# Kernel optimization log

Measured on AMD Instinct MI355X. Metric: run time of the kernel, lower is better.

Reference implementation:

```python
import jax, jax.numpy as jnp
import numpy as np

B, T, D = 8, 2048, 512


def setup_inputs() -> dict:
    key = jax.random.key(0)
    ks = jax.random.split(key, 12)
    s = 1.0 / np.sqrt(D)
    return {
        "x": jax.random.normal(ks[0], (B, T, D), dtype=jnp.float32),
        "Wq": jax.random.normal(ks[1], (D, D), dtype=jnp.float32) * s,
        "bq": jax.random.normal(ks[2], (D,), dtype=jnp.float32) * 0.01,
        "Wk": jax.random.normal(ks[3], (D, D), dtype=jnp.float32) * s,
        "bk": jax.random.normal(ks[4], (D,), dtype=jnp.float32) * 0.01,
        "Wv": jax.random.normal(ks[5], (D, D), dtype=jnp.float32) * s,
        "bv": jax.random.normal(ks[6], (D,), dtype=jnp.float32) * 0.01,
        "Wbeta": jax.random.normal(ks[7], (1, D), dtype=jnp.float32) * s,
        "bbeta": jax.random.normal(ks[8], (1,), dtype=jnp.float32) * 0.01,
        "Wo": jax.random.normal(ks[9], (D, D), dtype=jnp.float32) * s,
        "bo": jax.random.normal(ks[10], (D,), dtype=jnp.float32) * 0.01,
    }


def _l2_normalize(v, eps=1e-12):
    # torch F.normalize(p=2, dim=-1): v / max(||v||, eps)
    n = jnp.sqrt(jnp.sum(v * v, axis=-1, keepdims=True))
    return v / jnp.maximum(n, eps)


def _deltanet(x, Wq, bq, Wk, bk, Wv, bv, Wbeta, bbeta, Wo, bo):
    Q = x @ Wq.T + bq                      # [B,T,D]
    K = _l2_normalize(x @ Wk.T + bk)       # [B,T,D], unit-norm keys
    V = x @ Wv.T + bv                      # [B,T,D]
    Beta = jax.nn.sigmoid(K @ Wbeta.T + bbeta)  # [B,T,1]

    # time-major for scan: [T,B,D] / [T,B,1]
    Qt = jnp.swapaxes(Q, 0, 1)
    Kt = jnp.swapaxes(K, 0, 1)
    Vt = jnp.swapaxes(V, 0, 1)
    Bt = jnp.swapaxes(Beta, 0, 1)

    S0 = jnp.zeros((x.shape[0], x.shape[-1], x.shape[-1]), dtype=x.dtype)

    def step(S, inp):
        q, k, v, beta = inp                 # [B,D],[B,D],[B,D],[B,1]
        Sk = jnp.einsum("bij,bj->bi", S, k)           # S k_t
        b = beta[:, :, None]                            # [B,1,1]
        # S_t = S - beta (S k) k^T + beta v k^T
        S = S - b * (Sk[:, :, None] * k[:, None, :]) + b * (v[:, :, None] * k[:, None, :])
        o = jnp.einsum("bij,bj->bi", S, q)              # o_t = S_t q_t
        return S, o

    _, Ot = jax.lax.scan(step, S0, (Qt, Kt, Vt, Bt))    # [T,B,D]
    O = jnp.swapaxes(Ot, 0, 1)                          # [B,T,D]
    return O @ Wo.T + bo


def reference(x, Wq, bq, Wk, bk, Wv, bv, Wbeta, bbeta, Wo, bo):
    return _deltanet(x, Wq, bq, Wk, bk, Wv, bv, Wbeta, bbeta, Wo, bo)
```

## Files before the change

### kernel.cpp

```cpp
#include <hip/hip_runtime.h>

#define D 512
#define T 2048
#define BATCH 8
#define M_ROWS (BATCH*T)
#define CHK 64
#define NCHB 32
#define NCHUNK 256

typedef __attribute__((ext_vector_type(8))) short short8;
typedef __attribute__((ext_vector_type(4))) float floatx4;

__device__ __forceinline__ unsigned short f2bf(float f) {
  unsigned int u = __float_as_uint(f);
  u += 0x7FFFu + ((u >> 16) & 1u);
  return (unsigned short)(u >> 16);
}
__device__ __forceinline__ float bf2f(unsigned int h) {
  return __uint_as_float(h << 16);
}
__device__ __forceinline__ float wave_allreduce(float v) {
  #pragma unroll
  for (int m = 32; m; m >>= 1) v += __shfl_xor(v, m, 64);
  return v;
}
__device__ __forceinline__ void unpack8(uint4 r, float f[8]) {
  f[0] = bf2f(r.x & 0xffffu); f[1] = bf2f(r.x >> 16);
  f[2] = bf2f(r.y & 0xffffu); f[3] = bf2f(r.y >> 16);
  f[4] = bf2f(r.z & 0xffffu); f[5] = bf2f(r.z >> 16);
  f[6] = bf2f(r.w & 0xffffu); f[7] = bf2f(r.w >> 16);
}

typedef const __attribute__((address_space(1))) void* gas_ptr;
typedef __attribute__((address_space(3))) void* lds_ptr;
__device__ __forceinline__ void gld16(const void* g, void* l) {
  __builtin_amdgcn_global_load_lds((gas_ptr)g, (lds_ptr)l, 16, 0, 0);
}

__global__ __launch_bounds__(256) void cast_kernel(const float* __restrict__ src,
                                                   unsigned short* __restrict__ dst, int n) {
  int idx = (blockIdx.x * 256 + threadIdx.x) * 8;
  if (idx >= n) return;
  const float4* sp = (const float4*)(src + idx);
  float4 a = sp[0], b = sp[1];
  uint4 o;
  o.x = f2bf(a.x) | ((unsigned)f2bf(a.y) << 16);
  o.y = f2bf(a.z) | ((unsigned)f2bf(a.w) << 16);
  o.z = f2bf(b.x) | ((unsigned)f2bf(b.y) << 16);
  o.w = f2bf(b.z) | ((unsigned)f2bf(b.w) << 16);
  *(uint4*)(dst + idx) = o;
}

#define BM 128
#define BN 128
#define BK 32

template<bool OUT_BF16>
__global__ __launch_bounds__(256) void gemm_nt(
    const unsigned short* __restrict__ A, const unsigned short* __restrict__ Bw,
    const float* __restrict__ bias, void* __restrict__ Cout, int M, int N, int K)
{
  __shared__ __align__(16) unsigned short As[BM * BK];
  __shared__ __align__(16) unsigned short Bs[BN * BK];
  int tid  = threadIdx.x;
  int lane = tid & 63;
  int wave = tid >> 6;
  int waveM = (wave >> 1) * 64;
  int waveN = (wave & 1) * 64;
  int lrow = lane & 15;
  int quad = lane >> 4;

  floatx4 acc[4][4];
  #pragma unroll
  for (int a_ = 0; a_ < 4; ++a_)
    #pragma unroll
    for (int b_ = 0; b_ < 4; ++b_) acc[a_][b_] = (floatx4){0.f, 0.f, 0.f, 0.f};

  const unsigned short* Ap = A  + (size_t)(blockIdx.y * BM) * K;
  const unsigned short* Bp = Bw + (size_t)(blockIdx.x * BN) * K;
  int r0 = tid >> 2;
  int c0 = (tid & 3) * 8;

  unsigned short* AsW = As + (wave << 9);
  unsigned short* BsW = Bs + (wave << 9);
  const unsigned short* ApL = Ap + (size_t)r0 * K + c0;
  const unsigned short* ApH = Ap + (size_t)(r0 + 64) * K + c0;
  const unsigned short* BpL = Bp + (size_t)r0 * K + c0;
  const unsigned short* BpH = Bp + (size_t)(r0 + 64) * K + c0;

  for (int k0 = 0; k0 < K; k0 += BK) {
    __syncthreads();
    gld16(ApL + k0, AsW);
    gld16(ApH + k0, AsW + 2048);
    gld16(BpL + k0, BsW);
    gld16(BpH + k0, BsW + 2048);
    __syncthreads();
    short8 af[4], bf[4];
    #pragma unroll
    for (int mt = 0; mt < 4; ++mt)
      af[mt] = *(const short8*)&As[(waveM + mt * 16 + lrow) * BK + quad * 8];
    #pragma unroll
    for (int nt = 0; nt < 4; ++nt)
      bf[nt] = *(const short8*)&Bs[(waveN + nt * 16 + lrow) * BK + quad * 8];
    #pragma unroll
    for (int mt = 0; mt < 4; ++mt)
      #pragma unroll
      for (int nt = 0; nt < 4; ++nt)
        acc[mt][nt] = __builtin_amdgcn_mfma_f32_16x16x32_bf16(af[mt], bf[nt], acc[mt][nt], 0, 0, 0);
  }

  int cm = blockIdx.y * BM + waveM;
  int cn = blockIdx.x * BN + waveN;
  #pragma unroll
  for (int nt = 0; nt < 4; ++nt) {
    int col = cn + nt * 16 + lrow;
    float bv = bias[col];
    #pragma unroll
    for (int mt = 0; mt < 4; ++mt) {
      #pragma unroll
      for (int r = 0; r < 4; ++r) {
        int row = cm + mt * 16 + quad * 4 + r;
        float v = acc[mt][nt][r] + bv;
        if (OUT_BF16) ((unsigned short*)Cout)[(size_t)row * N + col] = f2bf(v);
        else          ((float*)Cout)[(size_t)row * N + col] = v;
      }
    }
  }
}

__global__ __launch_bounds__(256) void norm_beta_kernel(
    unsigned short* __restrict__ Kb, const float* __restrict__ Wbeta,
    const float* __restrict__ bbeta, float* __restrict__ Beta)
{
  int w = blockIdx.x * 4 + (threadIdx.x >> 6);
  int lane = threadIdx.x & 63;
  unsigned short* kp = Kb + (size_t)w * D + lane * 8;
  uint4 raw = *(uint4*)kp;
  float kv[8]; unpack8(raw, kv);
  float ss = 0.f;
  #pragma unroll
  for (int m = 0; m < 8; ++m) ss += kv[m] * kv[m];
  ss = wave_allreduce(ss);
  float inv = 1.0f / fmaxf(sqrtf(ss), 1e-12f);
  const float* wb = Wbeta + lane * 8;
  float dotp = 0.f;
  #pragma unroll
  for (int m = 0; m < 8; ++m) { kv[m] *= inv; dotp += kv[m] * wb[m]; }
  uint4 o;
  o.x = f2bf(kv[0]) | ((unsigned)f2bf(kv[1]) << 16);
  o.y = f2bf(kv[2]) | ((unsigned)f2bf(kv[3]) << 16);
  o.z = f2bf(kv[4]) | ((unsigned)f2bf(kv[5]) << 16);
  o.w = f2bf(kv[6]) | ((unsigned)f2bf(kv[7]) << 16);
  *(uint4*)kp = o;
  dotp = wave_allreduce(dotp);
  if (lane == 0) Beta[w] = 1.0f / (1.0f + expf(-(dotp + bbeta[0])));
}

__global__ __launch_bounds__(256) void transpose_kv(
    const unsigned short* __restrict__ Kb, const unsigned short* __restrict__ Vb,
    unsigned short* __restrict__ KT, unsigned short* __restrict__ VT)
{
  __shared__ __align__(16) unsigned short Kc[64 * 520];
  int cb = blockIdx.x & 255, tid = threadIdx.x;
  const unsigned short* src = (blockIdx.x < 256 ? Kb : Vb) + (size_t)cb * 64 * 512;
  unsigned short* dst = (blockIdx.x < 256 ? KT : VT) + (size_t)cb * 32768;
  #pragma unroll
  for (int it = 0; it < 16; ++it) {
    int e = it * 2048 + tid * 8;
    int row = e >> 9, col = e & 511;
    *(uint4*)&Kc[row * 520 + col] = *(const uint4*)&src[row * 512 + col];
  }
  __syncthreads();
  #pragma unroll
  for (int it = 0; it < 16; ++it) {
    int e = it * 2048 + tid * 8;
    int dk = e >> 6, t0 = e & 63;
    uint4 o;
    unsigned short tv[8];
    #pragma unroll
    for (int u = 0; u < 8; ++u) tv[u] = Kc[(t0 + u) * 520 + dk];
    o.x = tv[0] | ((unsigned)tv[1] << 16);
    o.y = tv[2] | ((unsigned)tv[3] << 16);
    o.z = tv[4] | ((unsigned)tv[5] << 16);
    o.w = tv[6] | ((unsigned)tv[7] << 16);
    *(uint4*)&dst[e] = o;
  }
}

__global__ __launch_bounds__(256) void gram_kernel(
    const unsigned short* __restrict__ Qb, const unsigned short* __restrict__ Kb,
    const float* __restrict__ Beta, float* __restrict__ Abuf,
    unsigned short* __restrict__ Msb)
{
  int cb = blockIdx.x, tid = threadIdx.x, lane = tid & 63, w = tid >> 6;
  int lr = lane & 15, quad = lane >> 4;
  const unsigned short* kc = Kb + (size_t)cb * 64 * 512;
  const unsigned short* qc = Qb + (size_t)cb * 64 * 512;
  floatx4 accK[4], accQ[4];
  #pragma unroll
  for (int nt = 0; nt < 4; ++nt) { accK[nt] = (floatx4){0,0,0,0}; accQ[nt] = (floatx4){0,0,0,0}; }
  #pragma unroll
  for (int ks = 0; ks < 16; ++ks) {
    short8 ak = *(const short8*)&kc[(w * 16 + lr) * 512 + ks * 32 + quad * 8];
    short8 aq = *(const short8*)&qc[(w * 16 + lr) * 512 + ks * 32 + quad * 8];
    short8 bk[4];
    #pragma unroll
    for (int nt = 0; nt < 4; ++nt)
      bk[nt] = *(const short8*)&kc[(nt * 16 + lr) * 512 + ks * 32 + quad * 8];
    #pragma unroll
    for (int nt = 0; nt < 4; ++nt) {
      accK[nt] = __builtin_amdgcn_mfma_f32_16x16x32_bf16(ak, bk[nt], accK[nt], 0, 0, 0);
      accQ[nt] = __builtin_amdgcn_mfma_f32_16x16x32_bf16(aq, bk[nt], accQ[nt], 0, 0, 0);
    }
  }
  #pragma unroll
  for (int nt = 0; nt < 4; ++nt)
    #pragma unroll
    for (int r = 0; r < 4; ++r) {
      int t = w * 16 + quad * 4 + r;
      int j = nt * 16 + lr;
      float bt = Beta[cb * 64 + t];
      Abuf[(size_t)cb * 4096 + t * 64 + j] = (j < t) ? bt * accK[nt][r] : 0.f;
      Msb[(size_t)cb * 4096 + t * 64 + j]  = f2bf((j <= t) ? accQ[nt][r] : 0.f);
    }
}

__global__ __launch_bounds__(64) void tinv_kernel(
    const float* __restrict__ Abuf, const float* __restrict__ Beta,
    unsigned short* __restrict__ Tib)
{
  __shared__ float XT[64 * 68];
  int lane = threadIdx.x;
  int cb = blockIdx.x;
  float bl = Beta[cb * 64 + lane];
  const float* Ab = Abuf + (size_t)cb * 4096;
  unsigned short* To = Tib + (size_t)cb * 4096;
  float* Xr = XT + lane * 68;
  #pragma unroll
  for (int j = 0; j < 68; j += 4) *(float4*)&Xr[j] = (float4){0.f,0.f,0.f,0.f};
  for (int t = 0; t < 64; ++t) {
    const float* Ar = Ab + t * 64;
    float p0 = 0.f, p1 = 0.f, p2 = 0.f, p3 = 0.f;
    for (int jb = 0; jb < t; jb += 4) {
      float4 xv = *(const float4*)&Xr[jb];
      float4 av = *(const float4*)&Ar[jb];
      p0 = fmaf(av.x, xv.x, p0); p1 = fmaf(av.y, xv.y, p1);
      p2 = fmaf(av.z, xv.z, p2); p3 = fmaf(av.w, xv.w, p3);
    }
    float y = ((lane == t) ? 1.f : 0.f) - (p0 + p1) - (p2 + p3);
    Xr[t] = y;
    To[t * 64 + lane] = f2bf(y * bl);
  }
}

__global__ __launch_bounds__(256) void wu_kernel(
    const unsigned short* __restrict__ Tib, const unsigned short* __restrict__ KT,
    const unsigned short* __restrict__ VT, unsigned short* __restrict__ Wneg,
    unsigned short* __restrict__ Ubar)
{
  __shared__ __align__(16) unsigned short WL[64 * 512];
  __shared__ __align__(16) unsigned short UL[64 * 512];
  int cb = blockIdx.x, tid = threadIdx.x, lane = tid & 63, w = tid >> 6;
  int lr = lane & 15, quad = lane >> 4;
  short8 af0 = *(const short8*)&Tib[(size_t)cb * 4096 + (w * 16 + lr) * 64 + quad * 8];
  short8 af1 = *(const short8*)&Tib[(size_t)cb * 4096 + (w * 16 + lr) * 64 + 32 + quad * 8];
  const unsigned short* ktc = KT + (size_t)cb * 32768 + lr * 64 + quad * 8;
  const unsigned short* vtc = VT + (size_t)cb * 32768 + lr * 64 + quad * 8;
  int tbase = w * 16 + quad * 4;
  #pragma unroll 4
  for (int nt = 0; nt < 32; ++nt) {
    short8 bk0 = *(const short8*)(ktc + nt * 1024);
    short8 bk1 = *(const short8*)(ktc + nt * 1024 + 32);
    short8 bv0 = *(const short8*)(vtc + nt * 1024);
    short8 bv1 = *(const short8*)(vtc + nt * 1024 + 32);
    floatx4 z = (floatx4){0.f,0.f,0.f,0.f};
    floatx4 aw = __builtin_amdgcn_mfma_f32_16x16x32_bf16(af0, bk0, z, 0, 0, 0);
    aw = __builtin_amdgcn_mfma_f32_16x16x32_bf16(af1, bk1, aw, 0, 0, 0);
    floatx4 au = __builtin_amdgcn_mfma_f32_16x16x32_bf16(af0, bv0, z, 0, 0, 0);
    au = __builtin_amdgcn_mfma_f32_16x16x32_bf16(af1, bv1, au, 0, 0, 0);
    int bi = nt * 2 + (lr >> 3);
    int lo = lr & 7;
    #pragma unroll
    for (int r = 0; r < 4; ++r) {
      int tt = tbase + r;
      int bis = bi ^ (tt & 7);
      WL[tt * 512 + bis * 8 + lo] = f2bf(-aw[r]);
      UL[tt * 512 + bis * 8 + lo] = f2bf(au[r]);
    }
  }
  __syncthreads();
  unsigned short* wd = Wneg + (size_t)cb * 32768;
  unsigned short* ud = Ubar + (size_t)cb * 32768;
  #pragma unroll
  for (int it = 0; it < 16; ++it) {
    int e = it * 2048 + tid * 8;
    int row = e >> 9, col = e & 511;
    int bis = (col >> 3) ^ (row & 7);
    *(uint4*)&wd[e] = *(const uint4*)&WL[row * 512 + bis * 8];
    *(uint4*)&ud[e] = *(const uint4*)&UL[row * 512 + bis * 8];
  }
}

__global__ __launch_bounds__(256, 1) void seq_kernel(
    const unsigned short* __restrict__ Wneg, const unsigned short* __restrict__ Qb,
    const unsigned short* __restrict__ Ubar, const unsigned short* __restrict__ Msb,
    const unsigned short* __restrict__ KT, unsigned short* __restrict__ Ob)
{
  __shared__ __align__(16) unsigned short Sb[16 * 520];
  __shared__ __align__(16) unsigned short Ut[16 * 72];
  int blk = blockIdx.x;
  int b = blk & 7, vs = blk >> 3;
  int vg0 = vs * 16;
  int tid = threadIdx.x, lane = tid & 63, w = tid >> 6;
  int lr = lane & 15, quad = lane >> 4;

  floatx4 sacc[8];
  #pragma unroll
  for (int nt = 0; nt < 8; ++nt) sacc[nt] = (floatx4){0.f,0.f,0.f,0.f};

  short8 wn[16], qf[16], kt[16], ms[2];
  unsigned short ub[4];

  auto LD_WQ = [&](int cb) {
    const unsigned short* wr = Wneg + ((size_t)cb * 64 + w * 16 + lr) * 512 + quad * 8;
    const unsigned short* qr = Qb   + ((size_t)cb * 64 + w * 16 + lr) * 512 + quad * 8;
    #pragma unroll
    for (int ks = 0; ks < 16; ++ks) {
      wn[ks] = *(const short8*)(wr + ks * 32);
      qf[ks] = *(const short8*)(qr + ks * 32);
    }
  };
  auto LD_KM = [&](int cb) {
    const unsigned short* kr = KT + (size_t)cb * 32768 + (w * 128 + lr) * 64 + quad * 8;
    #pragma unroll
    for (int nt = 0; nt < 8; ++nt) {
      kt[nt * 2 + 0] = *(const short8*)(kr + nt * 1024);
      kt[nt * 2 + 1] = *(const short8*)(kr + nt * 1024 + 32);
    }
    const unsigned short* mr = Msb + (size_t)cb * 4096 + (w * 16 + lr) * 64 + quad * 8;
    ms[0] = *(const short8*)(mr);
    ms[1] = *(const short8*)(mr + 32);
  };
  auto LD_UB = [&](int cb) {
    const unsigned short* ur = Ubar + ((size_t)cb * 64 + w * 16 + quad * 4) * 512 + vg0 + lr;
    #pragma unroll
    for (int r = 0; r < 4; ++r) ub[r] = ur[r * 512];
  };

  int cb0 = b * NCHB;
  LD_WQ(cb0); LD_KM(cb0); LD_UB(cb0);

  for (int ch = 0; ch < NCHB; ++ch) {
    int cb = cb0 + ch;
    int cbn = cb0 + (ch + 1 < NCHB ? ch + 1 : ch);
    #pragma unroll
    for (int nt = 0; nt < 8; ++nt)
      #pragma unroll
      for (int r = 0; r < 4; ++r)
        Sb[(quad * 4 + r) * 520 + w * 128 + nt * 16 + lr] = f2bf(sacc[nt][r]);
    __syncthreads();
    floatx4 du0, du1, do0, do1;
    #pragma unroll
    for (int r = 0; r < 4; ++r) du0[r] = bf2f(ub[r]);
    du1 = (floatx4){0.f,0.f,0.f,0.f};
    do0 = (floatx4){0.f,0.f,0.f,0.f};
    do1 = (floatx4){0.f,0.f,0.f,0.f};
    #pragma unroll
    for (int ks = 0; ks < 16; ++ks) {
      short8 sb = *(const short8*)&Sb[lr * 520 + ks * 32 + quad * 8];
      if (ks & 1) {
        du1 = __builtin_amdgcn_mfma_f32_16x16x32_bf16(wn[ks], sb, du1, 0, 0, 0);
        do1 = __builtin_amdgcn_mfma_f32_16x16x32_bf16(qf[ks], sb, do1, 0, 0, 0);
      } else {
        du0 = __builtin_amdgcn_mfma_f32_16x16x32_bf16(wn[ks], sb, du0, 0, 0, 0);
        do0 = __builtin_amdgcn_mfma_f32_16x16x32_bf16(qf[ks], sb, do0, 0, 0, 0);
      }
    }
    #pragma unroll
    for (int r = 0; r < 4; ++r)
      Ut[lr * 72 + w * 16 + quad * 4 + r] = f2bf(du0[r] + du1[r]);
    LD_WQ(cbn);
    LD_UB(cbn);
    __syncthreads();
    short8 a2_0 = *(const short8*)&Ut[lr * 72 + quad * 8];
    short8 a2_1 = *(const short8*)&Ut[lr * 72 + 32 + quad * 8];
    do0 = __builtin_amdgcn_mfma_f32_16x16x32_bf16(ms[0], a2_0, do0, 0, 0, 0);
    do1 = __builtin_amdgcn_mfma_f32_16x16x32_bf16(ms[1], a2_1, do1, 0, 0, 0);
    #pragma unroll
    for (int nt = 0; nt < 8; ++nt) {
      sacc[nt] = __builtin_amdgcn_mfma_f32_16x16x32_bf16(a2_0, kt[nt * 2 + 0], sacc[nt], 0, 0, 0);
      sacc[nt] = __builtin_amdgcn_mfma_f32_16x16x32_bf16(a2_1, kt[nt * 2 + 1], sacc[nt], 0, 0, 0);
    }
    {
      unsigned short* ob = Ob + ((size_t)cb * 64 + w * 16 + quad * 4) * 512 + vg0 + lr;
      #pragma unroll
      for (int r = 0; r < 4; ++r) ob[r * 512] = f2bf(do0[r] + do1[r]);
    }
    LD_KM(cbn);
  }
}

extern "C" void kernel_launch(void* const* d_in, const int* in_sizes, int n_in,
                              void* d_out, int out_size, void* d_ws, size_t ws_size,
                              hipStream_t stream) {
  const float* x     = (const float*)d_in[0];
  const float* Wq    = (const float*)d_in[1];
  const float* bq    = (const float*)d_in[2];
  const float* Wk    = (const float*)d_in[3];
  const float* bk    = (const float*)d_in[4];
  const float* Wv    = (const float*)d_in[5];
  const float* bv    = (const float*)d_in[6];
  const float* Wbeta = (const float*)d_in[7];
  const float* bbeta = (const float*)d_in[8];
  const float* Wo    = (const float*)d_in[9];
  const float* bo    = (const float*)d_in[10];

  const size_t NE = (size_t)M_ROWS * D;
  const size_t DD = (size_t)D * D;
  unsigned short* Qb  = (unsigned short*)d_ws;
  unsigned short* Kb  = Qb + NE;
  unsigned short* Vb  = Kb + NE;
  unsigned short* Xb  = Vb + NE;
  unsigned short* Wqb = Xb + NE;
  unsigned short* Wkb = Wqb + DD;
  unsigned short* Wvb = Wkb + DD;
  unsigned short* Wob = Wvb + DD;
  float* Beta = (float*)(Wob + DD);
  unsigned short* KT  = (unsigned short*)(Beta + M_ROWS);
  float* Abuf = (float*)(KT + NE);
  unsigned short* Msb = (unsigned short*)(Abuf + (size_t)NCHUNK * 4096);
  unsigned short* Tib = Msb + (size_t)NCHUNK * 4096;
  unsigned short* VT  = Tib + (size_t)NCHUNK * 4096;

  cast_kernel<<<(int)(NE / 2048), 256, 0, stream>>>(x, Xb, (int)NE);
  cast_kernel<<<(int)(DD / 2048), 256, 0, stream>>>(Wq, Wqb, (int)DD);
  cast_kernel<<<(int)(DD / 2048), 256, 0, stream>>>(Wk, Wkb, (int)DD);
  cast_kernel<<<(int)(DD / 2048), 256, 0, stream>>>(Wv, Wvb, (int)DD);
  cast_kernel<<<(int)(DD / 2048), 256, 0, stream>>>(Wo, Wob, (int)DD);

  dim3 gg(D / BN, M_ROWS / BM);
  gemm_nt<true><<<gg, 256, 0, stream>>>(Xb, Wqb, bq, Qb, M_ROWS, D, D);
  gemm_nt<true><<<gg, 256, 0, stream>>>(Xb, Wkb, bk, Kb, M_ROWS, D, D);
  gemm_nt<true><<<gg, 256, 0, stream>>>(Xb, Wvb, bv, Vb, M_ROWS, D, D);

  norm_beta_kernel<<<M_ROWS / 4, 256, 0, stream>>>(Kb, Wbeta, bbeta, Beta);

  transpose_kv<<<2 * NCHUNK, 256, 0, stream>>>(Kb, Vb, KT, VT);
  gram_kernel<<<NCHUNK, 256, 0, stream>>>(Qb, Kb, Beta, Abuf, Msb);
  tinv_kernel<<<NCHUNK, 64, 0, stream>>>(Abuf, Beta, Tib);
  wu_kernel<<<NCHUNK, 256, 0, stream>>>(Tib, KT, VT, Xb, Kb);

  seq_kernel<<<NCHUNK, 256, 0, stream>>>(Xb, Qb, Kb, Msb, KT, Vb);

  gemm_nt<false><<<gg, 256, 0, stream>>>(Vb, Wob, bo, (float*)d_out, M_ROWS, D, D);
}
```

Baseline: 474.5 us.

## Stage Wneg and transposed K through swizzled LDS in sequential kernel

The sequential scan kernel no longer keeps the Wneg and K^T chunk fragments in registers. It copies them asynchronously from global memory into LDS with gld16, and the copy for the next chunk overlaps the current chunk's MFMAs. To make the LDS reads bank-conflict free, K^T is written with an XOR swizzle in transpose_kv, and Wneg/Ubar keep the swizzled layout from wu_kernel. Consumers (wu_kernel's K loads and seq_kernel's Ubar loads) index accordingly. This frees many VGPRs and spreads global loads across the loop, at the cost of about 146KB of LDS and relying on correct completion waits for the async copies.

```diff
diff --git a/kernel.cpp b/kernel.cpp
--- a/kernel.cpp
+++ b/kernel.cpp
@@ -162,8 +162,9 @@
 {
   __shared__ __align__(16) unsigned short Kc[64 * 520];
   int cb = blockIdx.x & 255, tid = threadIdx.x;
-  const unsigned short* src = (blockIdx.x < 256 ? Kb : Vb) + (size_t)cb * 64 * 512;
-  unsigned short* dst = (blockIdx.x < 256 ? KT : VT) + (size_t)cb * 32768;
+  bool isK = blockIdx.x < 256;
+  const unsigned short* src = (isK ? Kb : Vb) + (size_t)cb * 64 * 512;
+  unsigned short* dst = (isK ? KT : VT) + (size_t)cb * 32768;
   #pragma unroll
   for (int it = 0; it < 16; ++it) {
     int e = it * 2048 + tid * 8;
@@ -183,7 +184,8 @@
     o.y = tv[2] | ((unsigned)tv[3] << 16);
     o.z = tv[4] | ((unsigned)tv[5] << 16);
     o.w = tv[6] | ((unsigned)tv[7] << 16);
-    *(uint4*)&dst[e] = o;
+    int bis = isK ? ((t0 >> 3) ^ (dk & 7)) : (t0 >> 3);
+    *(uint4*)&dst[(dk << 6) + bis * 8] = o;
   }
 }
 
@@ -261,16 +263,18 @@
   __shared__ __align__(16) unsigned short WL[64 * 512];
   __shared__ __align__(16) unsigned short UL[64 * 512];
   int cb = blockIdx.x, tid = threadIdx.x, lane = tid & 63, w = tid >> 6;
-  int lr = lane & 15, quad = lane >> 4;
+  int lr = lane & 15, quad = lane >> 4, lrx = lr & 7;
   short8 af0 = *(const short8*)&Tib[(size_t)cb * 4096 + (w * 16 + lr) * 64 + quad * 8];
   short8 af1 = *(const short8*)&Tib[(size_t)cb * 4096 + (w * 16 + lr) * 64 + 32 + quad * 8];
-  const unsigned short* ktc = KT + (size_t)cb * 32768 + lr * 64 + quad * 8;
+  const unsigned short* ktc = KT + (size_t)cb * 32768 + lr * 64;
   const unsigned short* vtc = VT + (size_t)cb * 32768 + lr * 64 + quad * 8;
+  int kc0 = (quad ^ lrx) * 8;
+  int kc1 = ((quad + 4) ^ lrx) * 8;
   int tbase = w * 16 + quad * 4;
   #pragma unroll 4
   for (int nt = 0; nt < 32; ++nt) {
-    short8 bk0 = *(const short8*)(ktc + nt * 1024);
-    short8 bk1 = *(const short8*)(ktc + nt * 1024 + 32);
+    short8 bk0 = *(const short8*)(ktc + nt * 1024 + kc0);
+    short8 bk1 = *(const short8*)(ktc + nt * 1024 + kc1);
     short8 bv0 = *(const short8*)(vtc + nt * 1024);
     short8 bv1 = *(const short8*)(vtc + nt * 1024 + 32);
     floatx4 z = (floatx4){0.f,0.f,0.f,0.f};
@@ -294,10 +298,8 @@
   #pragma unroll
   for (int it = 0; it < 16; ++it) {
     int e = it * 2048 + tid * 8;
-    int row = e >> 9, col = e & 511;
-    int bis = (col >> 3) ^ (row & 7);
-    *(uint4*)&wd[e] = *(const uint4*)&WL[row * 512 + bis * 8];
-    *(uint4*)&ud[e] = *(const uint4*)&UL[row * 512 + bis * 8];
+    *(uint4*)&wd[e] = *(const uint4*)&WL[e];
+    *(uint4*)&ud[e] = *(const uint4*)&UL[e];
   }
 }
 
@@ -306,49 +308,58 @@
     const unsigned short* __restrict__ Ubar, const unsigned short* __restrict__ Msb,
     const unsigned short* __restrict__ KT, unsigned short* __restrict__ Ob)
 {
+  __shared__ __align__(16) unsigned short WnegL[64 * 512];
+  __shared__ __align__(16) unsigned short KTL[512 * 64];
   __shared__ __align__(16) unsigned short Sb[16 * 520];
   __shared__ __align__(16) unsigned short Ut[16 * 72];
   int blk = blockIdx.x;
   int b = blk & 7, vs = blk >> 3;
   int vg0 = vs * 16;
   int tid = threadIdx.x, lane = tid & 63, w = tid >> 6;
-  int lr = lane & 15, quad = lane >> 4;
+  int lr = lane & 15, quad = lane >> 4, lrx = lr & 7;
 
   floatx4 sacc[8];
   #pragma unroll
   for (int nt = 0; nt < 8; ++nt) sacc[nt] = (floatx4){0.f,0.f,0.f,0.f};
 
-  short8 wn[16], qf[16], kt[16], ms[2];
+  short8 qf[16], ms[2];
   unsigned short ub[4];
 
-  auto LD_WQ = [&](int cb) {
-    const unsigned short* wr = Wneg + ((size_t)cb * 64 + w * 16 + lr) * 512 + quad * 8;
-    const unsigned short* qr = Qb   + ((size_t)cb * 64 + w * 16 + lr) * 512 + quad * 8;
-    #pragma unroll
-    for (int ks = 0; ks < 16; ++ks) {
-      wn[ks] = *(const short8*)(wr + ks * 32);
-      qf[ks] = *(const short8*)(qr + ks * 32);
-    }
+  auto STAGE_W = [&](int cb) {
+    const unsigned short* src = Wneg + (size_t)cb * 32768 + w * 8192 + lane * 8;
+    unsigned short* dst = WnegL + w * 8192;
+    #pragma unroll
+    for (int j = 0; j < 16; ++j) gld16(src + j * 512, dst + j * 512);
   };
-  auto LD_KM = [&](int cb) {
-    const unsigned short* kr = KT + (size_t)cb * 32768 + (w * 128 + lr) * 64 + quad * 8;
-    #pragma unroll
-    for (int nt = 0; nt < 8; ++nt) {
-      kt[nt * 2 + 0] = *(const short8*)(kr + nt * 1024);
-      kt[nt * 2 + 1] = *(const short8*)(kr + nt * 1024 + 32);
-    }
+  auto STAGE_K2 = [&](int cb, int nt) {
+    const unsigned short* src = KT + (size_t)cb * 32768 + w * 8192 + nt * 1024 + lane * 8;
+    unsigned short* dst = KTL + w * 8192 + nt * 1024;
+    gld16(src, dst);
+    gld16(src + 512, dst + 512);
+  };
+  auto LD_Q = [&](int cb) {
+    const unsigned short* qr = Qb + ((size_t)cb * 64 + w * 16 + lr) * 512 + quad * 8;
+    #pragma unroll
+    for (int ks = 0; ks < 16; ++ks) qf[ks] = *(const short8*)(qr + ks * 32);
+  };
+  auto LD_MS = [&](int cb) {
     const unsigned short* mr = Msb + (size_t)cb * 4096 + (w * 16 + lr) * 64 + quad * 8;
     ms[0] = *(const short8*)(mr);
     ms[1] = *(const short8*)(mr + 32);
   };
   auto LD_UB = [&](int cb) {
-    const unsigned short* ur = Ubar + ((size_t)cb * 64 + w * 16 + quad * 4) * 512 + vg0 + lr;
-    #pragma unroll
-    for (int r = 0; r < 4; ++r) ub[r] = ur[r * 512];
+    #pragma unroll
+    for (int r = 0; r < 4; ++r) {
+      int t = w * 16 + quad * 4 + r;
+      ub[r] = Ubar[((size_t)cb * 64 + t) * 512 + ((vg0 + lr) ^ ((t & 7) * 8))];
+    }
   };
 
   int cb0 = b * NCHB;
-  LD_WQ(cb0); LD_KM(cb0); LD_UB(cb0);
+  STAGE_W(cb0);
+  #pragma unroll
+  for (int nt = 0; nt < 8; ++nt) STAGE_K2(cb0, nt);
+  LD_Q(cb0); LD_MS(cb0); LD_UB(cb0);
 
   for (int ch = 0; ch < NCHB; ++ch) {
     int cb = cb0 + ch;
@@ -367,36 +378,40 @@
     do1 = (floatx4){0.f,0.f,0.f,0.f};
     #pragma unroll
     for (int ks = 0; ks < 16; ++ks) {
+      short8 wn = *(const short8*)&WnegL[(w * 16 + lr) * 512 + ((ks * 32 + quad * 8) ^ (lrx * 8))];
       short8 sb = *(const short8*)&Sb[lr * 520 + ks * 32 + quad * 8];
       if (ks & 1) {
-        du1 = __builtin_amdgcn_mfma_f32_16x16x32_bf16(wn[ks], sb, du1, 0, 0, 0);
+        du1 = __builtin_amdgcn_mfma_f32_16x16x32_bf16(wn, sb, du1, 0, 0, 0);
         do1 = __builtin_amdgcn_mfma_f32_16x16x32_bf16(qf[ks], sb, do1, 0, 0, 0);
       } else {
-        du0 = __builtin_amdgcn_mfma_f32_16x16x32_bf16(wn[ks], sb, du0, 0, 0, 0);
+        du0 = __builtin_amdgcn_mfma_f32_16x16x32_bf16(wn, sb, du0, 0, 0, 0);
         do0 = __builtin_amdgcn_mfma_f32_16x16x32_bf16(qf[ks], sb, do0, 0, 0, 0);
       }
     }
     #pragma unroll
     for (int r = 0; r < 4; ++r)
       Ut[lr * 72 + w * 16 + quad * 4 + r] = f2bf(du0[r] + du1[r]);
-    LD_WQ(cbn);
-    LD_UB(cbn);
     __syncthreads();
     short8 a2_0 = *(const short8*)&Ut[lr * 72 + quad * 8];
     short8 a2_1 = *(const short8*)&Ut[lr * 72 + 32 + quad * 8];
     do0 = __builtin_amdgcn_mfma_f32_16x16x32_bf16(ms[0], a2_0, do0, 0, 0, 0);
     do1 = __builtin_amdgcn_mfma_f32_16x16x32_bf16(ms[1], a2_1, do1, 0, 0, 0);
+    STAGE_W(cbn);
+    LD_Q(cbn); LD_MS(cbn); LD_UB(cbn);
     #pragma unroll
     for (int nt = 0; nt < 8; ++nt) {
-      sacc[nt] = __builtin_amdgcn_mfma_f32_16x16x32_bf16(a2_0, kt[nt * 2 + 0], sacc[nt], 0, 0, 0);
-      sacc[nt] = __builtin_amdgcn_mfma_f32_16x16x32_bf16(a2_1, kt[nt * 2 + 1], sacc[nt], 0, 0, 0);
+      int rb = (w * 128 + nt * 16 + lr) * 64;
+      short8 kt0 = *(const short8*)&KTL[rb + ((quad ^ lrx) * 8)];
+      short8 kt1 = *(const short8*)&KTL[rb + (((quad + 4) ^ lrx) * 8)];
+      sacc[nt] = __builtin_amdgcn_mfma_f32_16x16x32_bf16(a2_0, kt0, sacc[nt], 0, 0, 0);
+      sacc[nt] = __builtin_amdgcn_mfma_f32_16x16x32_bf16(a2_1, kt1, sacc[nt], 0, 0, 0);
+      STAGE_K2(cbn, nt);
     }
     {
       unsigned short* ob = Ob + ((size_t)cb * 64 + w * 16 + quad * 4) * 512 + vg0 + lr;
       #pragma unroll
       for (int r = 0; r < 4; ++r) ob[r * 512] = f2bf(do0[r] + do1[r]);
     }
-    LD_KM(cbn);
   }
 }
 
```

New measurement: 479.9 us. Within noise of the previous version (+1.1%).

## Split seq_kernel into U-waves and output waves with 512 threads per block

Applied to the files above, without the earlier changes.

Doubles the sequential chunk-scan block from 4 to 8 waves. Waves 0-3 compute the U correction and update the state, while waves 4-7 compute the Q·S output term and apply the intra-chunk mask product. Each wave now holds one 16-fragment operand set instead of two, which cuts register pressure, and the per-chunk MFMA chain is split across more waves to shorten the serial critical path. In exchange there are more waves per barrier, the Sb/Ut handoff in shared memory needs more coordination, and register budgets are tighter with launch bounds of 512 threads.

```diff
diff --git a/kernel.cpp b/kernel.cpp
--- a/kernel.cpp
+++ b/kernel.cpp
@@ -301,7 +301,7 @@
   }
 }
 
-__global__ __launch_bounds__(256, 1) void seq_kernel(
+__global__ __launch_bounds__(512, 2) void seq_kernel(
     const unsigned short* __restrict__ Wneg, const unsigned short* __restrict__ Qb,
     const unsigned short* __restrict__ Ubar, const unsigned short* __restrict__ Msb,
     const unsigned short* __restrict__ KT, unsigned short* __restrict__ Ob)
@@ -311,32 +311,34 @@
   int blk = blockIdx.x;
   int b = blk & 7, vs = blk >> 3;
   int vg0 = vs * 16;
-  int tid = threadIdx.x, lane = tid & 63, w = tid >> 6;
+  int tid = threadIdx.x, lane = tid & 63, wv = tid >> 6;
+  int w = wv & 3;
+  bool isU = (wv < 4);
   int lr = lane & 15, quad = lane >> 4;
 
   floatx4 sacc[8];
   #pragma unroll
   for (int nt = 0; nt < 8; ++nt) sacc[nt] = (floatx4){0.f,0.f,0.f,0.f};
 
-  short8 wn[16], qf[16], kt[16], ms[2];
+  short8 pf[16];
+  short8 kt[16];
+  short8 ms[2];
   unsigned short ub[4];
 
-  auto LD_WQ = [&](int cb) {
-    const unsigned short* wr = Wneg + ((size_t)cb * 64 + w * 16 + lr) * 512 + quad * 8;
-    const unsigned short* qr = Qb   + ((size_t)cb * 64 + w * 16 + lr) * 512 + quad * 8;
-    #pragma unroll
-    for (int ks = 0; ks < 16; ++ks) {
-      wn[ks] = *(const short8*)(wr + ks * 32);
-      qf[ks] = *(const short8*)(qr + ks * 32);
-    }
+  auto LD_PF = [&](int cb) {
+    const unsigned short* pr = (isU ? Wneg : Qb) + ((size_t)cb * 64 + w * 16 + lr) * 512 + quad * 8;
+    #pragma unroll
+    for (int ks = 0; ks < 16; ++ks) pf[ks] = *(const short8*)(pr + ks * 32);
   };
-  auto LD_KM = [&](int cb) {
+  auto LD_KT = [&](int cb) {
     const unsigned short* kr = KT + (size_t)cb * 32768 + (w * 128 + lr) * 64 + quad * 8;
     #pragma unroll
     for (int nt = 0; nt < 8; ++nt) {
       kt[nt * 2 + 0] = *(const short8*)(kr + nt * 1024);
       kt[nt * 2 + 1] = *(const short8*)(kr + nt * 1024 + 32);
     }
+  };
+  auto LD_MS = [&](int cb) {
     const unsigned short* mr = Msb + (size_t)cb * 4096 + (w * 16 + lr) * 64 + quad * 8;
     ms[0] = *(const short8*)(mr);
     ms[1] = *(const short8*)(mr + 32);
@@ -348,55 +350,66 @@
   };
 
   int cb0 = b * NCHB;
-  LD_WQ(cb0); LD_KM(cb0); LD_UB(cb0);
+  if (isU) { LD_PF(cb0); LD_KT(cb0); LD_UB(cb0); }
+  else     { LD_PF(cb0); LD_MS(cb0); }
 
   for (int ch = 0; ch < NCHB; ++ch) {
     int cb = cb0 + ch;
     int cbn = cb0 + (ch + 1 < NCHB ? ch + 1 : ch);
-    #pragma unroll
-    for (int nt = 0; nt < 8; ++nt)
-      #pragma unroll
-      for (int r = 0; r < 4; ++r)
-        Sb[(quad * 4 + r) * 520 + w * 128 + nt * 16 + lr] = f2bf(sacc[nt][r]);
+    if (isU) {
+      #pragma unroll
+      for (int nt = 0; nt < 8; ++nt)
+        #pragma unroll
+        for (int r = 0; r < 4; ++r)
+          Sb[(quad * 4 + r) * 520 + w * 128 + nt * 16 + lr] = f2bf(sacc[nt][r]);
+    }
     __syncthreads();
-    floatx4 du0, du1, do0, do1;
-    #pragma unroll
-    for (int r = 0; r < 4; ++r) du0[r] = bf2f(ub[r]);
-    du1 = (floatx4){0.f,0.f,0.f,0.f};
-    do0 = (floatx4){0.f,0.f,0.f,0.f};
-    do1 = (floatx4){0.f,0.f,0.f,0.f};
+    floatx4 d0, d1, d2, d3;
+    d0 = (floatx4){0.f,0.f,0.f,0.f};
+    if (isU) {
+      #pragma unroll
+      for (int r = 0; r < 4; ++r) d0[r] = bf2f(ub[r]);
+    }
+    d1 = (floatx4){0.f,0.f,0.f,0.f};
+    d2 = (floatx4){0.f,0.f,0.f,0.f};
+    d3 = (floatx4){0.f,0.f,0.f,0.f};
     #pragma unroll
     for (int ks = 0; ks < 16; ++ks) {
       short8 sb = *(const short8*)&Sb[lr * 520 + ks * 32 + quad * 8];
-      if (ks & 1) {
-        du1 = __builtin_amdgcn_mfma_f32_16x16x32_bf16(wn[ks], sb, du1, 0, 0, 0);
-        do1 = __builtin_amdgcn_mfma_f32_16x16x32_bf16(qf[ks], sb, do1, 0, 0, 0);
-      } else {
-        du0 = __builtin_amdgcn_mfma_f32_16x16x32_bf16(wn[ks], sb, du0, 0, 0, 0);
-        do0 = __builtin_amdgcn_mfma_f32_16x16x32_bf16(qf[ks], sb, do0, 0, 0, 0);
+      switch (ks & 3) {
+        case 0: d0 = __builtin_amdgcn_mfma_f32_16x16x32_bf16(pf[ks], sb, d0, 0, 0, 0); break;
+        case 1: d1 = __builtin_amdgcn_mfma_f32_16x16x32_bf16(pf[ks], sb, d1, 0, 0, 0); break;
+        case 2: d2 = __builtin_amdgcn_mfma_f32_16x16x32_bf16(pf[ks], sb, d2, 0, 0, 0); break;
+        default:d3 = __builtin_amdgcn_mfma_f32_16x16x32_bf16(pf[ks], sb, d3, 0, 0, 0); break;
       }
     }
-    #pragma unroll
-    for (int r = 0; r < 4; ++r)
-      Ut[lr * 72 + w * 16 + quad * 4 + r] = f2bf(du0[r] + du1[r]);
-    LD_WQ(cbn);
-    LD_UB(cbn);
+    if (isU) {
+      #pragma unroll
+      for (int r = 0; r < 4; ++r)
+        Ut[lr * 72 + w * 16 + quad * 4 + r] = f2bf(d0[r] + d1[r] + d2[r] + d3[r]);
+    }
     __syncthreads();
     short8 a2_0 = *(const short8*)&Ut[lr * 72 + quad * 8];
     short8 a2_1 = *(const short8*)&Ut[lr * 72 + 32 + quad * 8];
-    do0 = __builtin_amdgcn_mfma_f32_16x16x32_bf16(ms[0], a2_0, do0, 0, 0, 0);
-    do1 = __builtin_amdgcn_mfma_f32_16x16x32_bf16(ms[1], a2_1, do1, 0, 0, 0);
-    #pragma unroll
-    for (int nt = 0; nt < 8; ++nt) {
-      sacc[nt] = __builtin_amdgcn_mfma_f32_16x16x32_bf16(a2_0, kt[nt * 2 + 0], sacc[nt], 0, 0, 0);
-      sacc[nt] = __builtin_amdgcn_mfma_f32_16x16x32_bf16(a2_1, kt[nt * 2 + 1], sacc[nt], 0, 0, 0);
-    }
-    {
+    if (isU) {
+      LD_PF(cbn);
+      LD_UB(cbn);
+      #pragma unroll
+      for (int nt = 0; nt < 8; ++nt) {
+        sacc[nt] = __builtin_amdgcn_mfma_f32_16x16x32_bf16(a2_0, kt[nt * 2 + 0], sacc[nt], 0, 0, 0);
+        sacc[nt] = __builtin_amdgcn_mfma_f32_16x16x32_bf16(a2_1, kt[nt * 2 + 1], sacc[nt], 0, 0, 0);
+      }
+      LD_KT(cbn);
+    } else {
+      floatx4 os = d0 + d1 + d2 + d3;
+      os = __builtin_amdgcn_mfma_f32_16x16x32_bf16(ms[0], a2_0, os, 0, 0, 0);
+      os = __builtin_amdgcn_mfma_f32_16x16x32_bf16(ms[1], a2_1, os, 0, 0, 0);
       unsigned short* ob = Ob + ((size_t)cb * 64 + w * 16 + quad * 4) * 512 + vg0 + lr;
       #pragma unroll
-      for (int r = 0; r < 4; ++r) ob[r * 512] = f2bf(do0[r] + do1[r]);
-    }
-    LD_KM(cbn);
+      for (int r = 0; r < 4; ++r) ob[r * 512] = f2bf(os[r]);
+      LD_PF(cbn);
+      LD_MS(cbn);
+    }
   }
 }
 
@@ -450,7 +463,7 @@
   tinv_kernel<<<NCHUNK, 64, 0, stream>>>(Abuf, Beta, Tib);
   wu_kernel<<<NCHUNK, 256, 0, stream>>>(Tib, KT, VT, Xb, Kb);
 
-  seq_kernel<<<NCHUNK, 256, 0, stream>>>(Xb, Qb, Kb, Msb, KT, Vb);
+  seq_kernel<<<NCHUNK, 512, 0, stream>>>(Xb, Qb, Kb, Msb, KT, Vb);
 
   gemm_nt<false><<<gg, 256, 0, stream>>>(Vb, Wob, bo, (float*)d_out, M_ROWS, D, D);
 }
```

Result: slower. 495.9 us (+4.5%).

## Run sequential chunk scan with one wave per block, removing barriers

Applied to the files above, without the earlier changes.

The sequential state-propagation kernel now uses a single 64-lane wavefront per block that holds the whole 16x512 state slice (32 accumulator tiles) and loops over all four 16-row token groups itself, replacing four cooperating waves. This removes both __syncthreads per chunk and the cross-wave LDS handoff. The cost is that software prefetching of the next chunk's operands is dropped, so loads now sit directly on the serial critical path. Register pressure also rises sharply, and only 256 waves run on the GPU.

```diff
diff --git a/kernel.cpp b/kernel.cpp
--- a/kernel.cpp
+++ b/kernel.cpp
@@ -301,7 +301,7 @@
   }
 }
 
-__global__ __launch_bounds__(256, 1) void seq_kernel(
+__global__ __launch_bounds__(64) void seq_kernel(
     const unsigned short* __restrict__ Wneg, const unsigned short* __restrict__ Qb,
     const unsigned short* __restrict__ Ubar, const unsigned short* __restrict__ Msb,
     const unsigned short* __restrict__ KT, unsigned short* __restrict__ Ob)
@@ -311,92 +311,85 @@
   int blk = blockIdx.x;
   int b = blk & 7, vs = blk >> 3;
   int vg0 = vs * 16;
-  int tid = threadIdx.x, lane = tid & 63, w = tid >> 6;
+  int lane = threadIdx.x;
   int lr = lane & 15, quad = lane >> 4;
 
-  floatx4 sacc[8];
-  #pragma unroll
-  for (int nt = 0; nt < 8; ++nt) sacc[nt] = (floatx4){0.f,0.f,0.f,0.f};
-
-  short8 wn[16], qf[16], kt[16], ms[2];
-  unsigned short ub[4];
-
-  auto LD_WQ = [&](int cb) {
-    const unsigned short* wr = Wneg + ((size_t)cb * 64 + w * 16 + lr) * 512 + quad * 8;
-    const unsigned short* qr = Qb   + ((size_t)cb * 64 + w * 16 + lr) * 512 + quad * 8;
-    #pragma unroll
-    for (int ks = 0; ks < 16; ++ks) {
-      wn[ks] = *(const short8*)(wr + ks * 32);
-      qf[ks] = *(const short8*)(qr + ks * 32);
-    }
-  };
-  auto LD_KM = [&](int cb) {
-    const unsigned short* kr = KT + (size_t)cb * 32768 + (w * 128 + lr) * 64 + quad * 8;
-    #pragma unroll
-    for (int nt = 0; nt < 8; ++nt) {
-      kt[nt * 2 + 0] = *(const short8*)(kr + nt * 1024);
-      kt[nt * 2 + 1] = *(const short8*)(kr + nt * 1024 + 32);
-    }
-    const unsigned short* mr = Msb + (size_t)cb * 4096 + (w * 16 + lr) * 64 + quad * 8;
-    ms[0] = *(const short8*)(mr);
-    ms[1] = *(const short8*)(mr + 32);
-  };
-  auto LD_UB = [&](int cb) {
-    const unsigned short* ur = Ubar + ((size_t)cb * 64 + w * 16 + quad * 4) * 512 + vg0 + lr;
-    #pragma unroll
-    for (int r = 0; r < 4; ++r) ub[r] = ur[r * 512];
-  };
+  floatx4 sacc[4][8];
+  #pragma unroll
+  for (int dkg = 0; dkg < 4; ++dkg)
+    #pragma unroll
+    for (int nt = 0; nt < 8; ++nt) sacc[dkg][nt] = (floatx4){0.f,0.f,0.f,0.f};
 
   int cb0 = b * NCHB;
-  LD_WQ(cb0); LD_KM(cb0); LD_UB(cb0);
-
   for (int ch = 0; ch < NCHB; ++ch) {
     int cb = cb0 + ch;
-    int cbn = cb0 + (ch + 1 < NCHB ? ch + 1 : ch);
-    #pragma unroll
-    for (int nt = 0; nt < 8; ++nt)
+    #pragma unroll
+    for (int dkg = 0; dkg < 4; ++dkg)
+      #pragma unroll
+      for (int nt = 0; nt < 8; ++nt)
+        #pragma unroll
+        for (int r = 0; r < 4; ++r)
+          Sb[(quad * 4 + r) * 520 + dkg * 128 + nt * 16 + lr] = f2bf(sacc[dkg][nt][r]);
+    short8 sbv[16];
+    #pragma unroll
+    for (int ks = 0; ks < 16; ++ks)
+      sbv[ks] = *(const short8*)&Sb[lr * 520 + ks * 32 + quad * 8];
+    floatx4 dov[4];
+    #pragma unroll
+    for (int tq = 0; tq < 4; ++tq) {
+      const unsigned short* wr = Wneg + ((size_t)cb * 64 + tq * 16 + lr) * 512 + quad * 8;
+      const unsigned short* qr = Qb   + ((size_t)cb * 64 + tq * 16 + lr) * 512 + quad * 8;
+      const unsigned short* ur = Ubar + ((size_t)cb * 64 + tq * 16 + quad * 4) * 512 + vg0 + lr;
+      floatx4 du0, du1, dq0, dq1;
+      #pragma unroll
+      for (int r = 0; r < 4; ++r) du0[r] = bf2f(ur[r * 512]);
+      du1 = (floatx4){0.f,0.f,0.f,0.f};
+      dq0 = (floatx4){0.f,0.f,0.f,0.f};
+      dq1 = (floatx4){0.f,0.f,0.f,0.f};
+      #pragma unroll
+      for (int ks = 0; ks < 16; ++ks) {
+        short8 wn = *(const short8*)(wr + ks * 32);
+        short8 qf = *(const short8*)(qr + ks * 32);
+        if (ks & 1) {
+          du1 = __builtin_amdgcn_mfma_f32_16x16x32_bf16(wn, sbv[ks], du1, 0, 0, 0);
+          dq1 = __builtin_amdgcn_mfma_f32_16x16x32_bf16(qf, sbv[ks], dq1, 0, 0, 0);
+        } else {
+          du0 = __builtin_amdgcn_mfma_f32_16x16x32_bf16(wn, sbv[ks], du0, 0, 0, 0);
+          dq0 = __builtin_amdgcn_mfma_f32_16x16x32_bf16(qf, sbv[ks], dq0, 0, 0, 0);
+        }
+      }
+      dov[tq] = dq0 + dq1;
       #pragma unroll
       for (int r = 0; r < 4; ++r)
-        Sb[(quad * 4 + r) * 520 + w * 128 + nt * 16 + lr] = f2bf(sacc[nt][r]);
-    __syncthreads();
-    floatx4 du0, du1, do0, do1;
-    #pragma unroll
-    for (int r = 0; r < 4; ++r) du0[r] = bf2f(ub[r]);
-    du1 = (floatx4){0.f,0.f,0.f,0.f};
-    do0 = (floatx4){0.f,0.f,0.f,0.f};
-    do1 = (floatx4){0.f,0.f,0.f,0.f};
-    #pragma unroll
-    for (int ks = 0; ks < 16; ++ks) {
-      short8 sb = *(const short8*)&Sb[lr * 520 + ks * 32 + quad * 8];
-      if (ks & 1) {
-        du1 = __builtin_amdgcn_mfma_f32_16x16x32_bf16(wn[ks], sb, du1, 0, 0, 0);
-        do1 = __builtin_amdgcn_mfma_f32_16x16x32_bf16(qf[ks], sb, do1, 0, 0, 0);
-      } else {
-        du0 = __builtin_amdgcn_mfma_f32_16x16x32_bf16(wn[ks], sb, du0, 0, 0, 0);
-        do0 = __builtin_amdgcn_mfma_f32_16x16x32_bf16(qf[ks], sb, do0, 0, 0, 0);
-      }
-    }
-    #pragma unroll
-    for (int r = 0; r < 4; ++r)
-      Ut[lr * 72 + w * 16 + quad * 4 + r] = f2bf(du0[r] + du1[r]);
-    LD_WQ(cbn);
-    LD_UB(cbn);
-    __syncthreads();
+        Ut[lr * 72 + tq * 16 + quad * 4 + r] = f2bf(du0[r] + du1[r]);
+    }
     short8 a2_0 = *(const short8*)&Ut[lr * 72 + quad * 8];
     short8 a2_1 = *(const short8*)&Ut[lr * 72 + 32 + quad * 8];
-    do0 = __builtin_amdgcn_mfma_f32_16x16x32_bf16(ms[0], a2_0, do0, 0, 0, 0);
-    do1 = __builtin_amdgcn_mfma_f32_16x16x32_bf16(ms[1], a2_1, do1, 0, 0, 0);
-    #pragma unroll
-    for (int nt = 0; nt < 8; ++nt) {
-      sacc[nt] = __builtin_amdgcn_mfma_f32_16x16x32_bf16(a2_0, kt[nt * 2 + 0], sacc[nt], 0, 0, 0);
-      sacc[nt] = __builtin_amdgcn_mfma_f32_16x16x32_bf16(a2_1, kt[nt * 2 + 1], sacc[nt], 0, 0, 0);
-    }
     {
-      unsigned short* ob = Ob + ((size_t)cb * 64 + w * 16 + quad * 4) * 512 + vg0 + lr;
-      #pragma unroll
-      for (int r = 0; r < 4; ++r) ob[r * 512] = f2bf(do0[r] + do1[r]);
-    }
-    LD_KM(cbn);
+      const unsigned short* kr = KT + (size_t)cb * 32768 + lr * 64 + quad * 8;
+      #pragma unroll
+      for (int dkg = 0; dkg < 4; ++dkg)
+        #pragma unroll
+        for (int nt = 0; nt < 8; ++nt) {
+          const unsigned short* kp = kr + (size_t)(dkg * 128 + nt * 16) * 64;
+          short8 k0 = *(const short8*)kp;
+          short8 k1 = *(const short8*)(kp + 32);
+          sacc[dkg][nt] = __builtin_amdgcn_mfma_f32_16x16x32_bf16(a2_0, k0, sacc[dkg][nt], 0, 0, 0);
+          sacc[dkg][nt] = __builtin_amdgcn_mfma_f32_16x16x32_bf16(a2_1, k1, sacc[dkg][nt], 0, 0, 0);
+        }
+    }
+    #pragma unroll
+    for (int tq = 0; tq < 4; ++tq) {
+      const unsigned short* mr = Msb + (size_t)cb * 4096 + (tq * 16 + lr) * 64 + quad * 8;
+      short8 m0 = *(const short8*)(mr);
+      short8 m1 = *(const short8*)(mr + 32);
+      floatx4 os = dov[tq];
+      os = __builtin_amdgcn_mfma_f32_16x16x32_bf16(m0, a2_0, os, 0, 0, 0);
+      os = __builtin_amdgcn_mfma_f32_16x16x32_bf16(m1, a2_1, os, 0, 0, 0);
+      unsigned short* ob = Ob + ((size_t)cb * 64 + tq * 16 + quad * 4) * 512 + vg0 + lr;
+      #pragma unroll
+      for (int r = 0; r < 4; ++r) ob[r * 512] = f2bf(os[r]);
+    }
   }
 }
 
@@ -450,7 +443,7 @@
   tinv_kernel<<<NCHUNK, 64, 0, stream>>>(Abuf, Beta, Tib);
   wu_kernel<<<NCHUNK, 256, 0, stream>>>(Tib, KT, VT, Xb, Kb);
 
-  seq_kernel<<<NCHUNK, 256, 0, stream>>>(Xb, Qb, Kb, Msb, KT, Vb);
+  seq_kernel<<<NCHUNK, 64, 0, stream>>>(Xb, Qb, Kb, Msb, KT, Vb);
 
   gemm_nt<false><<<gg, 256, 0, stream>>>(Vb, Wob, bo, (float*)d_out, M_ROWS, D, D);
 }
```

After: 923.5 us. 1.95x slower.
